# Performance work log

Measured on AMD Instinct MI355X. Metric: run time of the kernel, lower is better.

## Reference

```python
import jax, jax.numpy as jnp
import numpy as np

N_NODES = 100000
N_EDGES = 1600000
D_IN, D_HID, D_OUT = 256, 512, 48
K_STEPS = 10
ALPHA = 0.1


def setup_inputs() -> dict:
    key = jax.random.key(0)
    k_x, k_e, k_w1, k_w2 = jax.random.split(key, 4)
    x = jax.random.normal(k_x, (N_NODES, D_IN), dtype=jnp.float32)
    edge_index = jax.random.randint(k_e, (2, N_EDGES), 0, N_NODES, dtype=jnp.int64)
    # MLP params (Kaiming-ish scaling)
    W1 = jax.random.normal(k_w1, (D_IN, D_HID), dtype=jnp.float32) * (1.0 / np.sqrt(D_IN))
    b1 = jnp.zeros((D_HID,), dtype=jnp.float32)
    W2 = jax.random.normal(k_w2, (D_HID, D_OUT), dtype=jnp.float32) * (1.0 / np.sqrt(D_HID))
    b2 = jnp.zeros((D_OUT,), dtype=jnp.float32)
    return {"x": x, "edge_index": edge_index, "W1": W1, "b1": b1, "W2": W2, "b2": b2}


def reference(x, edge_index, W1, b1, W2, b2):
    N = x.shape[0]
    # --- MLP encoder ---
    h = jax.nn.relu(x @ W1 + b1) @ W2 + b2  # [N, D_OUT]

    # --- APPNP propagation (PyG defaults: add self-loops, symmetric gcn_norm) ---
    loop = jnp.arange(N, dtype=edge_index.dtype)
    src = jnp.concatenate([edge_index[0], loop])  # [E+N]
    dst = jnp.concatenate([edge_index[1], loop])
    ones = jnp.ones(src.shape[0], dtype=h.dtype)
    deg = jax.ops.segment_sum(ones, dst, num_segments=N)  # in-degree incl. self-loop
    dinv = jnp.where(deg > 0, jax.lax.rsqrt(deg), 0.0)
    norm = dinv[src] * dinv[dst]  # [E+N]

    out = h
    for _ in range(K_STEPS):
        msg = out[src] * norm[:, None]                      # gather + scale
        agg = jax.ops.segment_sum(msg, dst, num_segments=N)  # scatter-add
        out = (1.0 - ALPHA) * agg + ALPHA * h                # teleport mix
    return out
```

## Files before the change

### kernel.cpp

```cpp
#include <hip/hip_runtime.h>
#include <hip/hip_fp16.h>

constexpr int D_IN = 256, D_HID = 512, D_OUT = 48;
constexpr int HPAD = 64;
constexpr int K_STEPS = 10;

typedef __attribute__((ext_vector_type(8))) __bf16 bf16x8;
typedef __attribute__((ext_vector_type(4))) float f32x4;

__device__ __forceinline__ unsigned short f2bf(float f) {
  unsigned u = __builtin_bit_cast(unsigned, f);
  u += 0x7fffu + ((u >> 16) & 1u);
  return (unsigned short)(u >> 16);
}

__device__ __forceinline__ void gl2lds16(const unsigned short* g, unsigned short* l) {
  __builtin_amdgcn_global_load_lds(
      (const __attribute__((address_space(1))) unsigned int*)g,
      (__attribute__((address_space(3))) unsigned int*)l, 16, 0, 0);
}


__global__ void zero1_kernel(int* __restrict__ a, int N) {
  int i = blockIdx.x * 256 + threadIdx.x;
  if (i < N) a[i] = 0;
}

__global__ __launch_bounds__(256) void count_kernel(const int* __restrict__ dst,
                                                    int* __restrict__ cnt,
                                                    int* __restrict__ rank, int E) {
  int e = blockIdx.x * 256 + threadIdx.x;
  if (e >= E) return;
  int d = __builtin_nontemporal_load(dst + e);
  int r = atomicAdd(&cnt[d], 1);
  __builtin_nontemporal_store(r, rank + e);
}

__global__ void dinv_kernel(const int* __restrict__ cnt, float* __restrict__ dinv, int N) {
  int n = blockIdx.x * 256 + threadIdx.x;
  if (n < N) dinv[n] = rsqrtf((float)(cnt[n] + 1));
}

__global__ void scan1_kernel(const int* __restrict__ cnt, int* __restrict__ row_ptr,
                             int* __restrict__ bsum, int N) {
  __shared__ int sd[256];
  int tid = threadIdx.x, b = blockIdx.x;
  int i0 = b * 1024 + tid * 4;
  int v[4];
#pragma unroll
  for (int m = 0; m < 4; ++m) v[m] = (i0 + m < N) ? ((cnt[i0 + m] + 4) & ~3) : 0;
  int s = v[0] + v[1] + v[2] + v[3];
  sd[tid] = s;
  __syncthreads();
  for (int off = 1; off < 256; off <<= 1) {
    int t = (tid >= off) ? sd[tid - off] : 0;
    __syncthreads();
    sd[tid] += t;
    __syncthreads();
  }
  int run = sd[tid] - s;
#pragma unroll
  for (int m = 0; m < 4; ++m) {
    if (i0 + m < N) row_ptr[i0 + m] = run;
    run += v[m];
  }
  if (tid == 255) bsum[b] = sd[255];
}

__global__ void scan2_kernel(const int* __restrict__ bsum, int* __restrict__ bofs,
                             int* __restrict__ row_ptr, int NB, int N) {
  __shared__ int sd[128];
  int tid = threadIdx.x;
  int v = (tid < NB) ? bsum[tid] : 0;
  sd[tid] = v;
  __syncthreads();
  for (int off = 1; off < 128; off <<= 1) {
    int t = (tid >= off) ? sd[tid - off] : 0;
    __syncthreads();
    sd[tid] += t;
    __syncthreads();
  }
  if (tid < NB) bofs[tid] = sd[tid] - v;
  if (tid == 127) row_ptr[N] = sd[127];
}

__global__ void scan3_kernel(int* __restrict__ row_ptr, const int* __restrict__ bofs, int N) {
  int b = blockIdx.x;
  if (b == 0) return;
  int add = bofs[b];
  int i0 = b * 1024 + threadIdx.x * 4;
#pragma unroll
  for (int m = 0; m < 4; ++m)
    if (i0 + m < N) row_ptr[i0 + m] += add;
}

__global__ __launch_bounds__(256) void fill_kernel(
    const int* __restrict__ src, const int* __restrict__ dst,
    const int* __restrict__ row_ptr, const int* __restrict__ rank,
    int* __restrict__ edges, int E) {
  int e = blockIdx.x * 256 + threadIdx.x;
  if (e >= E) return;
  int d = __builtin_nontemporal_load(dst + e);
  int s = __builtin_nontemporal_load(src + e);
  int r = __builtin_nontemporal_load(rank + e);
  edges[row_ptr[d] + r] = s;
}

__global__ void pad_kernel(const int* __restrict__ cnt, const int* __restrict__ row_ptr,
                           int* __restrict__ edges, int N) {
  int n = blockIdx.x * 256 + threadIdx.x;
  if (n >= N) return;
  int a = row_ptr[n] + cnt[n];
  int b = row_ptr[n + 1];
  edges[a] = n;
  for (int p = a + 1; p < b; ++p) edges[p] = N;
}

__global__ void zrow_kernel(__half* __restrict__ a, __half* __restrict__ b, int N) {
  int t = threadIdx.x;
  a[(size_t)N * HPAD + t] = __float2half(0.f);
  b[(size_t)N * HPAD + t] = __float2half(0.f);
}


__global__ void convert_w1(const float* __restrict__ W1, unsigned short* __restrict__ W1F) {
  int i = blockIdx.x * 256 + threadIdx.x;
  if (i >= D_HID * D_IN) return;
  int c = i >> 8, k = i & 255;
  int ct = c >> 6, tn = (c >> 4) & 3, l15 = c & 15;
  int kb = k >> 5, q = (k >> 3) & 3, j = k & 7;
  int lane = (q << 4) | l15;
  int dst = (((ct * 4 + tn) * 8 + kb) << 9) + lane * 8 + j;
  W1F[dst] = f2bf(W1[k * D_HID + c]);
}

__global__ void convert_w2(const float* __restrict__ W2, unsigned short* __restrict__ W2F) {
  int i = blockIdx.x * 256 + threadIdx.x;
  if (i >= D_OUT * D_HID) return;
  int n = i >> 9, k = i & 511;
  int ct = k >> 6, kk = (k >> 5) & 1, q = (k >> 3) & 3, j = k & 7;
  int tn = n >> 4, l15 = n & 15;
  int lane = (q << 4) | l15;
  int dst = (((ct * 2 + kk) * 3 + tn) << 9) + lane * 8 + j;
  W2F[dst] = f2bf(W2[k * D_OUT + n]);
}


__global__ __launch_bounds__(512, 2) void encoder_kernel(
    const float* __restrict__ x, const float* __restrict__ b1,
    const float* __restrict__ b2, const float* __restrict__ dinvp,
    const unsigned short* __restrict__ W1F,
    const unsigned short* __restrict__ W2F,
    __half* __restrict__ h2, __half* __restrict__ qb, int N) {
  __shared__ unsigned short sW1[16384];
  __shared__ unsigned short sHid[8][16][72];
  __shared__ float sB1[512];
  __shared__ float sB2[64];

  int tid = threadIdx.x;
  int w = tid >> 6, lane = tid & 63;
  int q = lane >> 4, l15 = lane & 15;
  const int nStrips = (N + 127) >> 7;

  auto stageCt = [&](int c) {
    const unsigned short* gsrc = W1F + ((size_t)c << 14) + (w << 9) + lane * 8;
    unsigned short* ldst = &sW1[w << 9];
#pragma unroll
    for (int i = 0; i < 4; ++i)
      gl2lds16(gsrc + (i << 12), ldst + (i << 12));
  };

  int strip = blockIdx.x;
  stageCt(0);
  sB1[tid] = b1[tid];
  if (tid < 48) sB2[tid] = b2[tid];

  float4 xv[16];
  {
    int grow = strip * 128 + w * 16 + l15;
    bool rok = grow < N;
    const float* xr = x + (size_t)grow * D_IN;
#pragma unroll
    for (int jb = 0; jb < 8; ++jb) {
      xv[2 * jb]     = rok ? *(const float4*)(xr + jb * 32 + q * 8)
                           : make_float4(0.f, 0.f, 0.f, 0.f);
      xv[2 * jb + 1] = rok ? *(const float4*)(xr + jb * 32 + q * 8 + 4)
                           : make_float4(0.f, 0.f, 0.f, 0.f);
    }
  }
  __syncthreads();

  for (;;) {
    int nxt = strip + 256;
    bool hasNext = nxt < nStrips;
    int ngrow = nxt * 128 + w * 16 + l15;
    bool nok = hasNext && (ngrow < N);
    const float* nxr = x + (size_t)ngrow * D_IN;

    uint4 axu[8];
#pragma unroll
    for (int jb = 0; jb < 8; ++jb) {
      union { uint4 u; unsigned short s[8]; } uu;
      float4 v0 = xv[2 * jb], v1 = xv[2 * jb + 1];
      uu.s[0] = f2bf(v0.x); uu.s[1] = f2bf(v0.y); uu.s[2] = f2bf(v0.z); uu.s[3] = f2bf(v0.w);
      uu.s[4] = f2bf(v1.x); uu.s[5] = f2bf(v1.y); uu.s[6] = f2bf(v1.z); uu.s[7] = f2bf(v1.w);
      axu[jb] = uu.u;
    }

    f32x4 hacc[3];
#pragma unroll
    for (int t = 0; t < 3; ++t)
#pragma unroll
      for (int r = 0; r < 4; ++r) hacc[t][r] = 0.f;

#pragma unroll
    for (int ct = 0; ct < 8; ++ct) {
      int c0 = ct * 64;
      f32x4 acc[4];
#pragma unroll
      for (int t = 0; t < 4; ++t)
#pragma unroll
        for (int r = 0; r < 4; ++r) acc[t][r] = 0.f;

      const unsigned short* sb = &sW1[lane * 8];
#pragma unroll
      for (int kb = 0; kb < 8; ++kb) {
        bf16x8 a = __builtin_bit_cast(bf16x8, axu[kb]);
        bf16x8 bq0 = *(const bf16x8*)(sb + (kb << 9));
        bf16x8 bq1 = *(const bf16x8*)(sb + (kb << 9) + 4096);
        bf16x8 bq2 = *(const bf16x8*)(sb + (kb << 9) + 8192);
        bf16x8 bq3 = *(const bf16x8*)(sb + (kb << 9) + 12288);
        acc[0] = __builtin_amdgcn_mfma_f32_16x16x32_bf16(a, bq0, acc[0], 0, 0, 0);
        acc[1] = __builtin_amdgcn_mfma_f32_16x16x32_bf16(a, bq1, acc[1], 0, 0, 0);
        acc[2] = __builtin_amdgcn_mfma_f32_16x16x32_bf16(a, bq2, acc[2], 0, 0, 0);
        acc[3] = __builtin_amdgcn_mfma_f32_16x16x32_bf16(a, bq3, acc[3], 0, 0, 0);
      }
#pragma unroll
      for (int tn = 0; tn < 4; ++tn) {
        int c = tn * 16 + l15;
        float bias = sB1[c0 + c];
#pragma unroll
        for (int rg = 0; rg < 4; ++rg) {
          float v = acc[tn][rg] + bias;
          v = v > 0.f ? v : 0.f;
          sHid[w][q * 4 + rg][c] = f2bf(v);
        }
      }
#pragma unroll
      for (int kk = 0; kk < 2; ++kk) {
        bf16x8 a0 = *(const bf16x8*)&sHid[w][l15][kk * 32 + q * 8];
        const unsigned short* w2b = W2F + (((ct * 2 + kk) * 3) << 9) + lane * 8;
#pragma unroll
        for (int tn = 0; tn < 3; ++tn) {
          bf16x8 b = *(const bf16x8*)(w2b + (tn << 9));
          hacc[tn] = __builtin_amdgcn_mfma_f32_16x16x32_bf16(a0, b, hacc[tn], 0, 0, 0);
        }
      }
      __syncthreads();
      if (ct < 7) stageCt(ct + 1);
      if (hasNext) {
        xv[2 * ct]     = nok ? *(const float4*)(nxr + ct * 32 + q * 8)
                             : make_float4(0.f, 0.f, 0.f, 0.f);
        xv[2 * ct + 1] = nok ? *(const float4*)(nxr + ct * 32 + q * 8 + 4)
                             : make_float4(0.f, 0.f, 0.f, 0.f);
      }
      __syncthreads();
    }

    int row0 = strip * 128 + w * 16;
    float dv[4];
#pragma unroll
    for (int rg = 0; rg < 4; ++rg) {
      int gr = row0 + q * 4 + rg;
      dv[rg] = (gr < N) ? dinvp[gr] : 0.f;
    }
#pragma unroll
    for (int tn = 0; tn < 3; ++tn) {
      int c = tn * 16 + l15;
      float bias = sB2[c];
#pragma unroll
      for (int rg = 0; rg < 4; ++rg) {
        int gr = row0 + q * 4 + rg;
        if (gr < N) {
          float val = hacc[tn][rg] + bias;
          h2[(size_t)gr * HPAD + c] = __float2half(val);
          qb[(size_t)gr * HPAD + c] = __float2half(dv[rg] * val);
        }
      }
    }
#pragma unroll
    for (int rg = 0; rg < 4; ++rg) {
      int gr = row0 + q * 4 + rg;
      if (gr < N) {
        h2[(size_t)gr * HPAD + 48 + l15] = __float2half(0.f);
        qb[(size_t)gr * HPAD + 48 + l15] = __float2half(0.f);
      }
    }

    if (!hasNext) break;
    strip = nxt;
    stageCt(0);
    __syncthreads();
  }
}


__global__ __launch_bounds__(256) void prop_kernel(
    const __half* __restrict__ cur, const __half* __restrict__ h2,
    const float* __restrict__ dinv, const int* __restrict__ row_ptr,
    const int* __restrict__ edges, __half* __restrict__ nxt,
    float* __restrict__ outf, int N, int last) {
  int wid = (blockIdx.x * 256 + threadIdx.x) >> 6;
  int lane = threadIdx.x & 63;
  int half = lane >> 5;
  int slot = (lane >> 3) & 3;
  int s = lane & 7;
  int node = wid * 2 + half;
  bool nok = node < N;
  int p0 = 0, p1 = 0;
  if (nok) { int2 pp = *(const int2*)(row_ptr + node); p0 = pp.x; p1 = pp.y; }
  int d = p1 - p0;
  int dmax = max(d, __shfl_xor(d, 32));
  int nb = dmax >> 2;

  float acc[8];
#pragma unroll
  for (int i = 0; i < 8; ++i) acc[i] = 0.f;

  int p = p0 + slot;
  int e0 = N, e1 = N, e2 = N, e3 = N;
  if (nb > 0) e0 = edges[p];
  if (nb > 1) e1 = edges[p + 4];
  if (nb > 2) e2 = edges[p + 8];
  if (nb > 3) e3 = edges[p + 12];
  int b = 0;
  for (; b + 4 <= nb; b += 4) {
    int n0 = N, n1 = N, n2 = N, n3 = N;
    if (b + 4 < nb) n0 = edges[p + 16];
    if (b + 5 < nb) n1 = edges[p + 20];
    if (b + 6 < nb) n2 = edges[p + 24];
    if (b + 7 < nb) n3 = edges[p + 28];
    int i0 = (p      < p1) ? e0 : N;
    int i1 = (p + 4  < p1) ? e1 : N;
    int i2 = (p + 8  < p1) ? e2 : N;
    int i3 = (p + 12 < p1) ? e3 : N;
    union { float4 f; __half2 h[4]; } u0, u1, u2, u3;
    u0.f = *(const float4*)(cur + ((size_t)i0 << 6) + s * 8);
    u1.f = *(const float4*)(cur + ((size_t)i1 << 6) + s * 8);
    u2.f = *(const float4*)(cur + ((size_t)i2 << 6) + s * 8);
    u3.f = *(const float4*)(cur + ((size_t)i3 << 6) + s * 8);
#pragma unroll
    for (int i = 0; i < 4; ++i) {
      float2 f0 = __half22float2(u0.h[i]);
      float2 f1 = __half22float2(u1.h[i]);
      float2 f2 = __half22float2(u2.h[i]);
      float2 f3 = __half22float2(u3.h[i]);
      acc[2 * i]     += (f0.x + f1.x) + (f2.x + f3.x);
      acc[2 * i + 1] += (f0.y + f1.y) + (f2.y + f3.y);
    }
    e0 = n0; e1 = n1; e2 = n2; e3 = n3; p += 16;
  }
  if (b < nb) {
    int i0 = (p < p1) ? e0 : N;
    union { float4 f; __half2 h[4]; } u0;
    u0.f = *(const float4*)(cur + ((size_t)i0 << 6) + s * 8);
#pragma unroll
    for (int i = 0; i < 4; ++i) {
      float2 f0 = __half22float2(u0.h[i]);
      acc[2 * i]     += f0.x;
      acc[2 * i + 1] += f0.y;
    }
  }
  if (b + 1 < nb) {
    int i1 = (p + 4 < p1) ? e1 : N;
    union { float4 f; __half2 h[4]; } u1;
    u1.f = *(const float4*)(cur + ((size_t)i1 << 6) + s * 8);
#pragma unroll
    for (int i = 0; i < 4; ++i) {
      float2 f1 = __half22float2(u1.h[i]);
      acc[2 * i]     += f1.x;
      acc[2 * i + 1] += f1.y;
    }
  }
  if (b + 2 < nb) {
    int i2 = (p + 8 < p1) ? e2 : N;
    union { float4 f; __half2 h[4]; } u2;
    u2.f = *(const float4*)(cur + ((size_t)i2 << 6) + s * 8);
#pragma unroll
    for (int i = 0; i < 4; ++i) {
      float2 f2 = __half22float2(u2.h[i]);
      acc[2 * i]     += f2.x;
      acc[2 * i + 1] += f2.y;
    }
  }
#pragma unroll
  for (int i = 0; i < 8; ++i) {
    acc[i] += __int_as_float(__builtin_amdgcn_ds_swizzle(__float_as_int(acc[i]), 0x201F));
    acc[i] += __int_as_float(__builtin_amdgcn_ds_swizzle(__float_as_int(acc[i]), 0x401F));
  }
  if ((lane & 24) != 0 || !nok) return;
  float di = dinv[node];
  size_t base = ((size_t)node << 6) + s * 8;
  union { float4 f; __half2 h[4]; } uh;
  uh.f = *(const float4*)(h2 + base);
  float outv[8];
#pragma unroll
  for (int i = 0; i < 4; ++i) {
    float2 hf = __half22float2(uh.h[i]);
    outv[2 * i]     = 0.9f * di * acc[2 * i]     + 0.1f * hf.x;
    outv[2 * i + 1] = 0.9f * di * acc[2 * i + 1] + 0.1f * hf.y;
  }
  if (last) {
    if (s < 6) {
      float* op = outf + (size_t)node * D_OUT + s * 8;
      *(float4*)op       = make_float4(outv[0], outv[1], outv[2], outv[3]);
      *(float4*)(op + 4) = make_float4(outv[4], outv[5], outv[6], outv[7]);
    }
  } else {
    union { uint4 u4; __half2 h[4]; } o;
#pragma unroll
    for (int i = 0; i < 4; ++i)
      o.h[i] = __floats2half2_rn(di * outv[2 * i], di * outv[2 * i + 1]);
    *(uint4*)(nxt + base) = o.u4;
  }
}


extern "C" void kernel_launch(void* const* d_in, const int* in_sizes, int n_in,
                              void* d_out, int out_size, void* d_ws, size_t ws_size,
                              hipStream_t stream) {
  (void)n_in; (void)out_size; (void)ws_size;
  const float* x  = (const float*)d_in[0];
  const int*   ei = (const int*)d_in[1];
  const float* W1 = (const float*)d_in[2];
  const float* b1 = (const float*)d_in[3];
  const float* W2 = (const float*)d_in[4];
  const float* b2 = (const float*)d_in[5];
  const int N = in_sizes[0] / D_IN;
  const int E = in_sizes[1] / 2;
  const int* e_src = ei;
  const int* e_dst = ei + E;

  char* ws = (char*)d_ws;
  size_t off = 0;
  auto take = [&](size_t bytes) -> char* {
    char* p = ws + off;
    off += (bytes + 511) & ~(size_t)511;
    return p;
  };
  int* cnt      = (int*)take((size_t)N * 4);
  float* dinv   = (float*)take((size_t)N * 4);
  int* row_ptr  = (int*)take((size_t)(N + 1) * 4);
  int* bsum     = (int*)take(1024);
  int* bofs     = (int*)take(1024);
  int* rank     = (int*)take((size_t)E * 4);
  int* edges    = (int*)take(((size_t)E + 4 * (size_t)N + 1024) * 4);
  unsigned short* W1F = (unsigned short*)take((size_t)D_IN * D_HID * 2);
  unsigned short* W2F = (unsigned short*)take((size_t)D_HID * D_OUT * 2);
  __half* h2    = (__half*)take((size_t)N * HPAD * 2);
  __half* bufA  = (__half*)take((size_t)(N + 1) * HPAD * 2);
  __half* bufB  = (__half*)d_out;
  float* outp   = (float*)d_out;

  int nb256 = (N + 255) / 256;
  int eb256 = (E + 255) / 256;
  int NB    = (N + 1023) / 1024;

  zero1_kernel<<<nb256, 256, 0, stream>>>(cnt, N);
  count_kernel<<<eb256, 256, 0, stream>>>(e_dst, cnt, rank, E);
  dinv_kernel<<<nb256, 256, 0, stream>>>(cnt, dinv, N);
  scan1_kernel<<<NB, 256, 0, stream>>>(cnt, row_ptr, bsum, N);
  scan2_kernel<<<1, 128, 0, stream>>>(bsum, bofs, row_ptr, NB, N);
  scan3_kernel<<<NB, 256, 0, stream>>>(row_ptr, bofs, N);
  fill_kernel<<<eb256, 256, 0, stream>>>(e_src, e_dst, row_ptr, rank, edges, E);
  pad_kernel<<<nb256, 256, 0, stream>>>(cnt, row_ptr, edges, N);
  zrow_kernel<<<1, 64, 0, stream>>>(bufA, bufB, N);

  convert_w1<<<(D_IN * D_HID + 255) / 256, 256, 0, stream>>>(W1, W1F);
  convert_w2<<<(D_HID * D_OUT + 255) / 256, 256, 0, stream>>>(W2, W2F);
  encoder_kernel<<<256, 512, 0, stream>>>(x, b1, b2, dinv, W1F, W2F, h2, bufB, N);

  int waves = (N + 1) / 2;
  int pblocks = (waves + 3) / 4;
  const __half* src = bufB;
  __half* dst = bufA;
  for (int it = 1; it <= K_STEPS; ++it) {
    int last = (it == K_STEPS);
    prop_kernel<<<pblocks, 256, 0, stream>>>(src, h2, dinv, row_ptr, edges,
                                             dst, outp, N, last);
    src = dst;
    dst = (dst == bufA) ? bufB : bufA;
  }
}
```

Before: 732.1 us.

## Replace persistent strip-loop encoder with one block per 128-row strip

The encoder is no longer a persistent kernel of 256 blocks looping over strips while prefetching the next strip's x rows. It now launches one block per 128-row strip (about 782 blocks), each loading its own x rows and staging the W1 chunks once. This drops the software prefetch of x and the extra register pressure in exchange for more blocks. Each block must also reload W1 from L2 per strip, and x loads are no longer overlapped with compute inside a block. The edges workspace padding is also enlarged slightly.

```diff
diff --git a/kernel.cpp b/kernel.cpp
--- a/kernel.cpp
+++ b/kernel.cpp
@@ -160,147 +160,126 @@
   int tid = threadIdx.x;
   int w = tid >> 6, lane = tid & 63;
   int q = lane >> 4, l15 = lane & 15;
-  const int nStrips = (N + 127) >> 7;
-
-  auto stageCt = [&](int c) {
-    const unsigned short* gsrc = W1F + ((size_t)c << 14) + (w << 9) + lane * 8;
+  int row0 = blockIdx.x * 128 + w * 16;
+
+  {
+    const unsigned short* gsrc = W1F + (w << 9) + lane * 8;
     unsigned short* ldst = &sW1[w << 9];
 #pragma unroll
     for (int i = 0; i < 4; ++i)
       gl2lds16(gsrc + (i << 12), ldst + (i << 12));
-  };
-
-  int strip = blockIdx.x;
-  stageCt(0);
+  }
   sB1[tid] = b1[tid];
   if (tid < 48) sB2[tid] = b2[tid];
 
+  int grow = row0 + l15;
+  bool rok = grow < N;
+  const float* xr = x + (size_t)grow * D_IN;
   float4 xv[16];
-  {
-    int grow = strip * 128 + w * 16 + l15;
-    bool rok = grow < N;
-    const float* xr = x + (size_t)grow * D_IN;
-#pragma unroll
-    for (int jb = 0; jb < 8; ++jb) {
-      xv[2 * jb]     = rok ? *(const float4*)(xr + jb * 32 + q * 8)
-                           : make_float4(0.f, 0.f, 0.f, 0.f);
-      xv[2 * jb + 1] = rok ? *(const float4*)(xr + jb * 32 + q * 8 + 4)
-                           : make_float4(0.f, 0.f, 0.f, 0.f);
-    }
-  }
+#pragma unroll
+  for (int jb = 0; jb < 8; ++jb) {
+    xv[2 * jb]     = rok ? *(const float4*)(xr + jb * 32 + q * 8)
+                         : make_float4(0.f, 0.f, 0.f, 0.f);
+    xv[2 * jb + 1] = rok ? *(const float4*)(xr + jb * 32 + q * 8 + 4)
+                         : make_float4(0.f, 0.f, 0.f, 0.f);
+  }
+  uint4 axu[8];
+#pragma unroll
+  for (int jb = 0; jb < 8; ++jb) {
+    union { uint4 u; unsigned short s[8]; } uu;
+    float4 v0 = xv[2 * jb], v1 = xv[2 * jb + 1];
+    uu.s[0] = f2bf(v0.x); uu.s[1] = f2bf(v0.y); uu.s[2] = f2bf(v0.z); uu.s[3] = f2bf(v0.w);
+    uu.s[4] = f2bf(v1.x); uu.s[5] = f2bf(v1.y); uu.s[6] = f2bf(v1.z); uu.s[7] = f2bf(v1.w);
+    axu[jb] = uu.u;
+  }
+
+  f32x4 hacc[3];
+#pragma unroll
+  for (int t = 0; t < 3; ++t)
+#pragma unroll
+    for (int r = 0; r < 4; ++r) hacc[t][r] = 0.f;
+
   __syncthreads();
 
-  for (;;) {
-    int nxt = strip + 256;
-    bool hasNext = nxt < nStrips;
-    int ngrow = nxt * 128 + w * 16 + l15;
-    bool nok = hasNext && (ngrow < N);
-    const float* nxr = x + (size_t)ngrow * D_IN;
-
-    uint4 axu[8];
-#pragma unroll
-    for (int jb = 0; jb < 8; ++jb) {
-      union { uint4 u; unsigned short s[8]; } uu;
-      float4 v0 = xv[2 * jb], v1 = xv[2 * jb + 1];
-      uu.s[0] = f2bf(v0.x); uu.s[1] = f2bf(v0.y); uu.s[2] = f2bf(v0.z); uu.s[3] = f2bf(v0.w);
-      uu.s[4] = f2bf(v1.x); uu.s[5] = f2bf(v1.y); uu.s[6] = f2bf(v1.z); uu.s[7] = f2bf(v1.w);
-      axu[jb] = uu.u;
-    }
-
-    f32x4 hacc[3];
-#pragma unroll
-    for (int t = 0; t < 3; ++t)
-#pragma unroll
-      for (int r = 0; r < 4; ++r) hacc[t][r] = 0.f;
-
-#pragma unroll
-    for (int ct = 0; ct < 8; ++ct) {
-      int c0 = ct * 64;
-      f32x4 acc[4];
-#pragma unroll
-      for (int t = 0; t < 4; ++t)
-#pragma unroll
-        for (int r = 0; r < 4; ++r) acc[t][r] = 0.f;
-
-      const unsigned short* sb = &sW1[lane * 8];
-#pragma unroll
-      for (int kb = 0; kb < 8; ++kb) {
-        bf16x8 a = __builtin_bit_cast(bf16x8, axu[kb]);
-        bf16x8 bq0 = *(const bf16x8*)(sb + (kb << 9));
-        bf16x8 bq1 = *(const bf16x8*)(sb + (kb << 9) + 4096);
-        bf16x8 bq2 = *(const bf16x8*)(sb + (kb << 9) + 8192);
-        bf16x8 bq3 = *(const bf16x8*)(sb + (kb << 9) + 12288);
-        acc[0] = __builtin_amdgcn_mfma_f32_16x16x32_bf16(a, bq0, acc[0], 0, 0, 0);
-        acc[1] = __builtin_amdgcn_mfma_f32_16x16x32_bf16(a, bq1, acc[1], 0, 0, 0);
-        acc[2] = __builtin_amdgcn_mfma_f32_16x16x32_bf16(a, bq2, acc[2], 0, 0, 0);
-        acc[3] = __builtin_amdgcn_mfma_f32_16x16x32_bf16(a, bq3, acc[3], 0, 0, 0);
+  for (int ct = 0; ct < 8; ++ct) {
+    int c0 = ct * 64;
+    f32x4 acc[4];
+#pragma unroll
+    for (int t = 0; t < 4; ++t)
+#pragma unroll
+      for (int r = 0; r < 4; ++r) acc[t][r] = 0.f;
+
+    const unsigned short* sb = &sW1[lane * 8];
+#pragma unroll
+    for (int kb = 0; kb < 8; ++kb) {
+      bf16x8 a = __builtin_bit_cast(bf16x8, axu[kb]);
+      bf16x8 bq0 = *(const bf16x8*)(sb + (kb << 9));
+      bf16x8 bq1 = *(const bf16x8*)(sb + (kb << 9) + 4096);
+      bf16x8 bq2 = *(const bf16x8*)(sb + (kb << 9) + 8192);
+      bf16x8 bq3 = *(const bf16x8*)(sb + (kb << 9) + 12288);
+      acc[0] = __builtin_amdgcn_mfma_f32_16x16x32_bf16(a, bq0, acc[0], 0, 0, 0);
+      acc[1] = __builtin_amdgcn_mfma_f32_16x16x32_bf16(a, bq1, acc[1], 0, 0, 0);
+      acc[2] = __builtin_amdgcn_mfma_f32_16x16x32_bf16(a, bq2, acc[2], 0, 0, 0);
+      acc[3] = __builtin_amdgcn_mfma_f32_16x16x32_bf16(a, bq3, acc[3], 0, 0, 0);
+    }
+#pragma unroll
+    for (int tn = 0; tn < 4; ++tn) {
+      int c = tn * 16 + l15;
+      float bias = sB1[c0 + c];
+#pragma unroll
+      for (int rg = 0; rg < 4; ++rg) {
+        float v = acc[tn][rg] + bias;
+        v = v > 0.f ? v : 0.f;
+        sHid[w][q * 4 + rg][c] = f2bf(v);
       }
-#pragma unroll
-      for (int tn = 0; tn < 4; ++tn) {
-        int c = tn * 16 + l15;
-        float bias = sB1[c0 + c];
-#pragma unroll
-        for (int rg = 0; rg < 4; ++rg) {
-          float v = acc[tn][rg] + bias;
-          v = v > 0.f ? v : 0.f;
-          sHid[w][q * 4 + rg][c] = f2bf(v);
-        }
+    }
+#pragma unroll
+    for (int kk = 0; kk < 2; ++kk) {
+      bf16x8 a0 = *(const bf16x8*)&sHid[w][l15][kk * 32 + q * 8];
+      const unsigned short* w2b = W2F + (((ct * 2 + kk) * 3) << 9) + lane * 8;
+#pragma unroll
+      for (int tn = 0; tn < 3; ++tn) {
+        bf16x8 b = *(const bf16x8*)(w2b + (tn << 9));
+        hacc[tn] = __builtin_amdgcn_mfma_f32_16x16x32_bf16(a0, b, hacc[tn], 0, 0, 0);
       }
-#pragma unroll
-      for (int kk = 0; kk < 2; ++kk) {
-        bf16x8 a0 = *(const bf16x8*)&sHid[w][l15][kk * 32 + q * 8];
-        const unsigned short* w2b = W2F + (((ct * 2 + kk) * 3) << 9) + lane * 8;
-#pragma unroll
-        for (int tn = 0; tn < 3; ++tn) {
-          bf16x8 b = *(const bf16x8*)(w2b + (tn << 9));
-          hacc[tn] = __builtin_amdgcn_mfma_f32_16x16x32_bf16(a0, b, hacc[tn], 0, 0, 0);
-        }
-      }
+    }
+    __syncthreads();
+    if (ct < 7) {
+      const unsigned short* gsrc = W1F + ((size_t)(ct + 1) << 14) + (w << 9) + lane * 8;
+      unsigned short* ldst = &sW1[w << 9];
+#pragma unroll
+      for (int i = 0; i < 4; ++i)
+        gl2lds16(gsrc + (i << 12), ldst + (i << 12));
       __syncthreads();
-      if (ct < 7) stageCt(ct + 1);
-      if (hasNext) {
-        xv[2 * ct]     = nok ? *(const float4*)(nxr + ct * 32 + q * 8)
-                             : make_float4(0.f, 0.f, 0.f, 0.f);
-        xv[2 * ct + 1] = nok ? *(const float4*)(nxr + ct * 32 + q * 8 + 4)
-                             : make_float4(0.f, 0.f, 0.f, 0.f);
-      }
-      __syncthreads();
-    }
-
-    int row0 = strip * 128 + w * 16;
-    float dv[4];
-#pragma unroll
-    for (int rg = 0; rg < 4; ++rg) {
-      int gr = row0 + q * 4 + rg;
-      dv[rg] = (gr < N) ? dinvp[gr] : 0.f;
-    }
-#pragma unroll
-    for (int tn = 0; tn < 3; ++tn) {
-      int c = tn * 16 + l15;
-      float bias = sB2[c];
-#pragma unroll
-      for (int rg = 0; rg < 4; ++rg) {
-        int gr = row0 + q * 4 + rg;
-        if (gr < N) {
-          float val = hacc[tn][rg] + bias;
-          h2[(size_t)gr * HPAD + c] = __float2half(val);
-          qb[(size_t)gr * HPAD + c] = __float2half(dv[rg] * val);
-        }
-      }
-    }
+    }
+  }
+  float dv[4];
+#pragma unroll
+  for (int rg = 0; rg < 4; ++rg) {
+    int gr = row0 + q * 4 + rg;
+    dv[rg] = (gr < N) ? dinvp[gr] : 0.f;
+  }
+#pragma unroll
+  for (int tn = 0; tn < 3; ++tn) {
+    int c = tn * 16 + l15;
+    float bias = sB2[c];
 #pragma unroll
     for (int rg = 0; rg < 4; ++rg) {
       int gr = row0 + q * 4 + rg;
       if (gr < N) {
-        h2[(size_t)gr * HPAD + 48 + l15] = __float2half(0.f);
-        qb[(size_t)gr * HPAD + 48 + l15] = __float2half(0.f);
+        float val = hacc[tn][rg] + bias;
+        h2[(size_t)gr * HPAD + c] = __float2half(val);
+        qb[(size_t)gr * HPAD + c] = __float2half(dv[rg] * val);
       }
     }
-
-    if (!hasNext) break;
-    strip = nxt;
-    stageCt(0);
-    __syncthreads();
+  }
+#pragma unroll
+  for (int rg = 0; rg < 4; ++rg) {
+    int gr = row0 + q * 4 + rg;
+    if (gr < N) {
+      h2[(size_t)gr * HPAD + 48 + l15] = __float2half(0.f);
+      qb[(size_t)gr * HPAD + 48 + l15] = __float2half(0.f);
+    }
   }
 }
 
@@ -454,7 +433,7 @@
   int* bsum     = (int*)take(1024);
   int* bofs     = (int*)take(1024);
   int* rank     = (int*)take((size_t)E * 4);
-  int* edges    = (int*)take(((size_t)E + 4 * (size_t)N + 1024) * 4);
+  int* edges    = (int*)take(((size_t)E + 4 * (size_t)N + 2048) * 4);
   unsigned short* W1F = (unsigned short*)take((size_t)D_IN * D_HID * 2);
   unsigned short* W2F = (unsigned short*)take((size_t)D_HID * D_OUT * 2);
   __half* h2    = (__half*)take((size_t)N * HPAD * 2);
@@ -478,7 +457,8 @@
 
   convert_w1<<<(D_IN * D_HID + 255) / 256, 256, 0, stream>>>(W1, W1F);
   convert_w2<<<(D_HID * D_OUT + 255) / 256, 256, 0, stream>>>(W2, W2F);
-  encoder_kernel<<<256, 512, 0, stream>>>(x, b1, b2, dinv, W1F, W2F, h2, bufB, N);
+  encoder_kernel<<<(N + 127) / 128, 512, 0, stream>>>(x, b1, b2, dinv, W1F, W2F,
+                                                      h2, bufB, N);
 
   int waves = (N + 1) / 2;
   int pblocks = (waves + 3) / 4;
```

After: 651.1 us. 1.12x faster.
